# Kernel optimization log

Measured on AMD Instinct MI355X. Metric: run time of the kernel, lower is better.

Reference implementation:

```python
import jax, jax.numpy as jnp
import numpy as np

N, E, D, H, C = 50000, 1600000, 256, 8, 32

def setup_inputs() -> dict:
    key = jax.random.key(0)
    ks = jax.random.split(key, 7)
    feat = jax.random.normal(ks[0], (N, D), dtype=jnp.float32)
    edge_weight = jax.random.uniform(ks[1], (E,), dtype=jnp.float32)
    W_lin = jax.random.normal(ks[2], (D, H * C), dtype=jnp.float32) * (1.0 / np.sqrt(D))
    att_l = jax.random.normal(ks[3], (1, H, C), dtype=jnp.float32) * (1.0 / np.sqrt(H))
    att_r = jax.random.normal(ks[4], (1, H, C), dtype=jnp.float32) * (1.0 / np.sqrt(H))
    W_res = jax.random.normal(ks[5], (D, H * C), dtype=jnp.float32) * (1.0 / np.sqrt(D))
    edge_index = jax.random.randint(ks[6], (2, E), 0, N, dtype=jnp.int32)
    return {"feat": feat, "edge_weight": edge_weight, "W_lin": W_lin,
            "att_l": att_l, "att_r": att_r, "W_res": W_res, "edge_index": edge_index}

def reference(feat, edge_weight, W_lin, att_l, att_r, W_res, edge_index):
    n_nodes = feat.shape[0]
    h, c = att_l.shape[1], att_l.shape[2]
    src, dst = edge_index[0], edge_index[1]
    # node projection: [N, H, C]
    x = (feat @ W_lin).reshape(n_nodes, h, c)
    alpha_l = (x * att_l).sum(-1)  # [N, H]
    alpha_r = (x * att_r).sum(-1)  # [N, H]
    # per-edge scores [E, H]
    alpha = alpha_l[src] + alpha_r[dst]
    alpha = edge_weight[:, None] * alpha
    alpha = jnp.where(alpha > 0, alpha, 0.2 * alpha)  # leaky_relu(0.2)
    # segment softmax over destination nodes
    amax = jax.lax.stop_gradient(jax.ops.segment_max(alpha, dst, num_segments=n_nodes))
    ex = jnp.exp(alpha - amax[dst])
    denom = jax.ops.segment_sum(ex, dst, num_segments=n_nodes)
    coeff = ex / (denom[dst] + 1e-16)  # [E, H]
    # weighted message aggregation
    msg = x[src] * coeff[:, :, None]  # [E, H, C]
    agg = jax.ops.segment_sum(msg, dst, num_segments=n_nodes)  # [N, H, C]
    out = jax.nn.elu(agg).reshape(n_nodes, h * c)
    out = out + feat @ W_res  # residual
    return out
```

## Files before the change

### kernel.cpp

```cpp
#include <hip/hip_runtime.h>
#include <stdint.h>

#define D_DIM 256
#define NPAD  640
#define NSH   8

typedef __bf16 bf16x8 __attribute__((ext_vector_type(8)));
typedef float  f32x4  __attribute__((ext_vector_type(4)));

__device__ __forceinline__ float bf2f(unsigned short u) {
  union { unsigned int i; float f; } cv; cv.i = ((unsigned int)u) << 16; return cv.f;
}
__device__ __forceinline__ unsigned short f2bf(float f) {
  union { float f; unsigned int i; } cv; cv.f = f;
  unsigned int i = cv.i;
  unsigned int lsb = (i >> 16) & 1u;
  i += 0x7fffu + lsb;
  return (unsigned short)(i >> 16);
}
__device__ __forceinline__ void gld16(const void* gptr, void* lptr) {
  __builtin_amdgcn_global_load_lds(
      (const __attribute__((address_space(1))) unsigned int*)gptr,
      (__attribute__((address_space(3))) unsigned int*)lptr, 16, 0, 0);
}

__global__ __launch_bounds__(256) void setup_fused(
    const float* __restrict__ feat, unsigned short* __restrict__ fb,
    const float* __restrict__ W_lin, const float* __restrict__ W_res,
    const float* __restrict__ att_l, const float* __restrict__ att_r,
    unsigned short* __restrict__ Bt, int nelem, int nb_hist, int nb_cvt,
    const int* __restrict__ dst, int* __restrict__ cntS, int* __restrict__ rank,
    int E, int Np) {
  int bid = blockIdx.x, t = threadIdx.x;
  if (bid < nb_hist) {
    int base = bid * 2048 + t;
    #pragma unroll
    for (int u = 0; u < 8; ++u) {
      int e = base + u * 256;
      if (e < E) {
        int d = dst[e];
        rank[e] = atomicAdd(&cntS[(e & (NSH - 1)) * Np + d], 1);
      }
    }
    return;
  }
  bid -= nb_hist;
  if (bid < nb_cvt) {
    int i = (bid * 256 + t) * 8;
    if (i >= nelem) return;
    float4 v0 = *(const float4*)(feat + i);
    float4 v1 = *(const float4*)(feat + i + 4);
    ushort4 a, b;
    a.x = f2bf(v0.x); a.y = f2bf(v0.y); a.z = f2bf(v0.z); a.w = f2bf(v0.w);
    b.x = f2bf(v1.x); b.y = f2bf(v1.y); b.z = f2bf(v1.z); b.w = f2bf(v1.w);
    *(ushort4*)(fb + i) = a;
    *(ushort4*)(fb + i + 4) = b;
  } else {
    int idx = (bid - nb_cvt) * 256 + t;
    int n = idx >> 8, k = idx & 255;
    float v = 0.f;
    if (n < 256) v = W_lin[k * 256 + n];
    else if (n < 512) v = W_res[k * 256 + (n - 256)];
    else if (n < 520) {
      int h = n - 512; float s = 0.f;
      #pragma unroll
      for (int c = 0; c < 32; ++c) s += W_lin[k * 256 + h * 32 + c] * att_l[h * 32 + c];
      v = s;
    } else if (n < 528) {
      int h = n - 520; float s = 0.f;
      #pragma unroll
      for (int c = 0; c < 32; ++c) s += W_lin[k * 256 + h * 32 + c] * att_r[h * 32 + c];
      v = s;
    }
    Bt[idx] = f2bf(v);
  }
}

__global__ __launch_bounds__(256) void scan_partial(const int* __restrict__ cntS,
                                                    int* __restrict__ bsum, int N, int Np) {
  __shared__ int s[256];
  int t = threadIdx.x;
  int i = blockIdx.x * 256 + t;
  int v = 0;
  if (i < N) {
    #pragma unroll
    for (int sh = 0; sh < NSH; ++sh) v += cntS[sh * Np + i];
  }
  s[t] = v;
  __syncthreads();
  for (int off = 128; off > 0; off >>= 1) {
    if (t < off) s[t] += s[t + off];
    __syncthreads();
  }
  if (t == 0) bsum[blockIdx.x] = s[0];
}

__global__ __launch_bounds__(256) void scan_apply(const int* __restrict__ cntS,
                                                  const int* __restrict__ bsum,
                                                  int* __restrict__ row_ptr,
                                                  int* __restrict__ soffA, int N, int Np) {
  __shared__ int red[256];
  __shared__ int s[256];
  int t = threadIdx.x;
  int b = blockIdx.x;
  int acc = 0;
  for (int j = t; j < b; j += 256) acc += bsum[j];
  red[t] = acc;
  __syncthreads();
  for (int off = 128; off > 0; off >>= 1) {
    if (t < off) red[t] += red[t + off];
    __syncthreads();
  }
  int base = red[0];

  int i = b * 256 + t;
  int c[NSH]; int v = 0;
  if (i < N) {
    #pragma unroll
    for (int sh = 0; sh < NSH; ++sh) { c[sh] = cntS[sh * Np + i]; v += c[sh]; }
  }
  s[t] = v;
  __syncthreads();
  for (int off = 1; off < 256; off <<= 1) {
    int u = (t >= off) ? s[t - off] : 0;
    __syncthreads();
    s[t] += u;
    __syncthreads();
  }
  int excl = base + s[t] - v;
  if (i < N) {
    row_ptr[i] = excl;
    int run = excl;
    #pragma unroll
    for (int sh = 0; sh < NSH; ++sh) { soffA[sh * Np + i] = run; run += c[sh]; }
    if (i == N - 1) row_ptr[N] = excl + v;
  }
}

__global__ __launch_bounds__(256) void gemm_kernel(
    const unsigned short* __restrict__ A,
    const unsigned short* __restrict__ Bt,
    float* __restrict__ out, unsigned short* __restrict__ xbf,
    float* __restrict__ alpha_l, float* __restrict__ alpha_r, int M, int gx) {
  __shared__ unsigned short As[128 * 64];
  __shared__ unsigned short Bs[128 * 64];

  int tid  = threadIdx.x;
  int w    = tid >> 6, lane = tid & 63;

  int nwg  = (int)gridDim.x;
  int q    = nwg >> 3, r = nwg & 7;
  int xcd  = (int)blockIdx.x & 7, j = (int)blockIdx.x >> 3;
  int wg   = (xcd < r ? xcd * (q + 1) : r * (q + 1) + (xcd - r) * q) + j;

  int nbn  = NPAD / 128;
  int bm   = (wg / nbn) * 128, bn = (wg % nbn) * 128;
  int wm   = (w & 1) * 64, wn = (w >> 1) * 64;
  int l16  = lane & 15, quad = lane >> 4;

  f32x4 acc[4][4] = {};

  int sr8     = lane >> 3;
  int koff_sw = (((lane & 7) ^ sr8) * 8);

  for (int k0 = 0; k0 < 256; k0 += 64) {
    #pragma unroll
    for (int jj = 0; jj < 4; ++jj) {
      int rbase = w * 32 + jj * 8;
      int rga = bm + rbase + sr8; if (rga > M - 1) rga = M - 1;
      gld16(A  + (size_t)rga * 256 + k0 + koff_sw, &As[rbase * 64]);
      gld16(Bt + (size_t)(bn + rbase + sr8) * 256 + k0 + koff_sw, &Bs[rbase * 64]);
    }
    __syncthreads();
    #pragma unroll
    for (int kk = 0; kk < 64; kk += 32) {
      bf16x8 a[4], b[4];
      #pragma unroll
      for (int mi = 0; mi < 4; ++mi) {
        int rr = wm + mi * 16 + l16;
        int col = (kk * 2 + quad * 16) ^ ((rr & 7) << 4);
        a[mi] = *(const bf16x8*)((const char*)&As[rr * 64] + col);
      }
      #pragma unroll
      for (int ni = 0; ni < 4; ++ni) {
        int rr = wn + ni * 16 + l16;
        int col = (kk * 2 + quad * 16) ^ ((rr & 7) << 4);
        b[ni] = *(const bf16x8*)((const char*)&Bs[rr * 64] + col);
      }
      #pragma unroll
      for (int mi = 0; mi < 4; ++mi)
        #pragma unroll
        for (int ni = 0; ni < 4; ++ni)
          acc[mi][ni] = __builtin_amdgcn_mfma_f32_16x16x32_bf16(a[mi], b[ni], acc[mi][ni], 0, 0, 0);
    }
    __syncthreads();
  }

  #pragma unroll
  for (int mi = 0; mi < 4; ++mi) {
    #pragma unroll
    for (int rr = 0; rr < 4; ++rr) {
      int row = bm + wm + mi * 16 + quad * 4 + rr;
      if (row >= M) continue;
      #pragma unroll
      for (int ni = 0; ni < 4; ++ni) {
        int n = bn + wn + ni * 16 + l16;
        float v = acc[mi][ni][rr];
        if (n < 256)      xbf[(size_t)row * 256 + n] = f2bf(v);
        else if (n < 512) out[(size_t)row * 256 + (n - 256)] = v;
        else if (n < 520) alpha_l[row * 8 + (n - 512)] = v;
        else if (n < 528) alpha_r[row * 8 + (n - 520)] = v;
      }
    }
  }
}

__global__ __launch_bounds__(256) void scatter_kernel(
    const int* __restrict__ eidx, const float* __restrict__ ew,
    const int* __restrict__ soffA, const int* __restrict__ rank,
    int2* __restrict__ pairs, int E, int Np) {
  int e = blockIdx.x * 256 + threadIdx.x;
  if (e < E) {
    int d = eidx[E + e];
    int pos = soffA[(e & (NSH - 1)) * Np + d] + rank[e];
    int2 p; p.x = eidx[e]; p.y = __float_as_int(ew[e]);
    pairs[pos] = p;
  }
}

__global__ __launch_bounds__(256) void agg_kernel(
    const int* __restrict__ row_ptr, const int2* __restrict__ pairs,
    const float* __restrict__ alpha_l, const float* __restrict__ alpha_r,
    const unsigned short* __restrict__ xbf, float* __restrict__ out,
    int node_base, int node_lim) {
  __shared__ float red[2][64][6];
  int nin  = threadIdx.x >> 7;
  int wv   = (threadIdx.x >> 6) & 1;
  int lane = threadIdx.x & 63;
  int node = node_base + blockIdx.x * 2 + nin;
  bool active = node < node_lim;
  int h  = lane >> 3;
  int cb = lane << 2;

  float l = 0.f, ac0 = 0.f, ac1 = 0.f, ac2 = 0.f, ac3 = 0.f;

  if (active) {
    int beg = row_ptr[node], end = row_ptr[node + 1];
    if (beg < end) {
      float arv = alpha_r[node * 8 + h];
      int last = end - 1;
      const unsigned short* xb = xbf + cb;
      for (int jg = beg + wv * 4; jg < end; jg += 8) {
        int2 q[4];
        #pragma unroll
        for (int u = 0; u < 4; ++u) {
          int t = jg + u; t = (t < last) ? t : last;
          q[u] = pairs[t];
        }
        float al[4];
        #pragma unroll
        for (int u = 0; u < 4; ++u) al[u] = alpha_l[(size_t)q[u].x * 8 + h];
        ushort4 xv[4];
        #pragma unroll
        for (int u = 0; u < 4; ++u)
          xv[u] = *(const ushort4*)(xb + ((size_t)q[u].x << 8));
        #pragma unroll
        for (int u = 0; u < 4; ++u) {
          float a = __int_as_float(q[u].y) * (al[u] + arv);
          a = (a > 0.f) ? a : 0.2f * a;
          float p = __expf(a);
          p = (jg + u < end) ? p : 0.f;
          l += p;
          ac0 = fmaf(p, bf2f(xv[u].x), ac0);
          ac1 = fmaf(p, bf2f(xv[u].y), ac1);
          ac2 = fmaf(p, bf2f(xv[u].z), ac2);
          ac3 = fmaf(p, bf2f(xv[u].w), ac3);
        }
      }
    }
  }

  if (wv == 1) {
    red[nin][lane][0] = l;
    red[nin][lane][1] = ac0; red[nin][lane][2] = ac1;
    red[nin][lane][3] = ac2; red[nin][lane][4] = ac3;
  }
  __syncthreads();
  if (active && wv == 0) {
    l   += red[nin][lane][0];
    ac0 += red[nin][lane][1]; ac1 += red[nin][lane][2];
    ac2 += red[nin][lane][3]; ac3 += red[nin][lane][4];
    float r = 1.0f / (l + 1e-16f);
    float o0 = ac0 * r, o1 = ac1 * r, o2 = ac2 * r, o3 = ac3 * r;
    o0 = (o0 > 0.f) ? o0 : expm1f(o0);
    o1 = (o1 > 0.f) ? o1 : expm1f(o1);
    o2 = (o2 > 0.f) ? o2 : expm1f(o2);
    o3 = (o3 > 0.f) ? o3 : expm1f(o3);
    float4* op = (float4*)(out + ((size_t)node << 8) + cb);
    float4 res = *op;
    res.x += o0; res.y += o1; res.z += o2; res.w += o3;
    *op = res;
  }
}

extern "C" void kernel_launch(void* const* d_in, const int* in_sizes, int n_in,
                              void* d_out, int out_size, void* d_ws, size_t ws_size,
                              hipStream_t stream) {
  const float* feat  = (const float*)d_in[0];
  const float* ew    = (const float*)d_in[1];
  const float* W_lin = (const float*)d_in[2];
  const float* att_l = (const float*)d_in[3];
  const float* att_r = (const float*)d_in[4];
  const float* W_res = (const float*)d_in[5];
  const int*   eidx  = (const int*)d_in[6];
  float* out = (float*)d_out;

  int N = in_sizes[0] / D_DIM;
  int E = in_sizes[1];
  int Np = (N + 255) & ~255;

  char* p = (char*)d_ws;
  auto alloc = [&](size_t bytes) {
    char* r = p; p += (bytes + 255) & ~(size_t)255; return r;
  };
  unsigned short* xbf  = (unsigned short*)alloc((size_t)N * 256 * 2);
  unsigned short* fb   = (unsigned short*)alloc((size_t)N * 256 * 2);
  float* alpha_l       = (float*)alloc((size_t)N * 8 * 4);
  float* alpha_r       = (float*)alloc((size_t)N * 8 * 4);
  unsigned short* Bt   = (unsigned short*)alloc((size_t)NPAD * D_DIM * 2);
  int*   row_ptr       = (int*)alloc((size_t)(N + 1) * 4);
  int*   cntS          = (int*)alloc((size_t)NSH * Np * 4);
  int*   soffA         = (int*)alloc((size_t)NSH * Np * 4);
  int*   rank          = (int*)alloc((size_t)E * 4);
  int*   bsum          = (int*)alloc(1024);
  int2*  pairs_sep     = (int2*)alloc((size_t)E * 8);
  bool sep_ok = ((size_t)((char*)(pairs_sep + E) - (char*)d_ws) <= ws_size);
  int2* pairs = sep_ok ? pairs_sep : (int2*)fb;

  int nb      = (N + 255) / 256;
  int nb_cvt  = (N * 256 / 8 + 255) / 256;
  int nb_prep = NPAD * D_DIM / 256;
  int nb_hist = (E + 2047) / 2048;
  int nb_scat = (E + 255) / 256;
  int gx = (N + 127) / 128;
  int gemm_blocks = gx * (NPAD / 128);

  hipMemsetAsync(cntS, 0, (size_t)NSH * Np * 4, stream);

  setup_fused<<<nb_hist + nb_cvt + nb_prep, 256, 0, stream>>>(
      feat, fb, W_lin, W_res, att_l, att_r, Bt, N * 256, nb_hist, nb_cvt,
      eidx + E, cntS, rank, E, Np);

  gemm_kernel<<<gemm_blocks, 256, 0, stream>>>(
      fb, Bt, out, xbf, alpha_l, alpha_r, N, gx);

  scan_partial<<<nb, 256, 0, stream>>>(cntS, bsum, N, Np);
  scan_apply<<<nb, 256, 0, stream>>>(cntS, bsum, row_ptr, soffA, N, Np);

  scatter_kernel<<<nb_scat, 256, 0, stream>>>(eidx, ew, soffA, rank, pairs, E, Np);

  int Nh = ((N / 2) + 1) & ~1;
  if (Nh > N) Nh = N;
  int blocksA = (Nh + 1) / 2;
  int blocksB = (N - Nh + 1) / 2;
  if (blocksA > 0)
    agg_kernel<<<blocksA, 256, 0, stream>>>(row_ptr, pairs, alpha_l, alpha_r, xbf, out, 0, Nh);
  if (blocksB > 0)
    agg_kernel<<<blocksB, 256, 0, stream>>>(row_ptr, pairs, alpha_l, alpha_r, xbf, out, Nh, N);
}
```

Before: 402.3 us.

## Move edge histogram into GEMM epilogue and merge split aggregation launches

The per-destination edge histogram (atomic counts and ranks) moves out of the setup kernel and runs at the end of each GEMM block, over a chunk of edges sized so the GEMM grid covers all edges. The atomic work can then overlap with the memory- and compute-bound GEMM tail instead of running as separate blocks ahead of it. The two half-range aggregation launches are also merged into one launch over all nodes, saving a launch. The risk is longer GEMM blocks, plus atomic traffic contending with the GEMM stores.

```diff
diff --git a/kernel.cpp b/kernel.cpp
--- a/kernel.cpp
+++ b/kernel.cpp
@@ -24,27 +24,12 @@
       (__attribute__((address_space(3))) unsigned int*)lptr, 16, 0, 0);
 }
 
-__global__ __launch_bounds__(256) void setup_fused(
+__global__ __launch_bounds__(256) void setup_cvt_prep(
     const float* __restrict__ feat, unsigned short* __restrict__ fb,
     const float* __restrict__ W_lin, const float* __restrict__ W_res,
     const float* __restrict__ att_l, const float* __restrict__ att_r,
-    unsigned short* __restrict__ Bt, int nelem, int nb_hist, int nb_cvt,
-    const int* __restrict__ dst, int* __restrict__ cntS, int* __restrict__ rank,
-    int E, int Np) {
+    unsigned short* __restrict__ Bt, int nelem, int nb_cvt) {
   int bid = blockIdx.x, t = threadIdx.x;
-  if (bid < nb_hist) {
-    int base = bid * 2048 + t;
-    #pragma unroll
-    for (int u = 0; u < 8; ++u) {
-      int e = base + u * 256;
-      if (e < E) {
-        int d = dst[e];
-        rank[e] = atomicAdd(&cntS[(e & (NSH - 1)) * Np + d], 1);
-      }
-    }
-    return;
-  }
-  bid -= nb_hist;
   if (bid < nb_cvt) {
     int i = (bid * 256 + t) * 8;
     if (i >= nelem) return;
@@ -141,7 +126,9 @@
     const unsigned short* __restrict__ A,
     const unsigned short* __restrict__ Bt,
     float* __restrict__ out, unsigned short* __restrict__ xbf,
-    float* __restrict__ alpha_l, float* __restrict__ alpha_r, int M, int gx) {
+    float* __restrict__ alpha_l, float* __restrict__ alpha_r, int M, int gx,
+    const int* __restrict__ dst, int* __restrict__ cntS, int* __restrict__ rank,
+    int E, int Np, int echunk) {
   __shared__ unsigned short As[128 * 64];
   __shared__ unsigned short Bs[128 * 64];
 
@@ -212,6 +199,13 @@
         else if (n < 528) alpha_r[row * 8 + (n - 520)] = v;
       }
     }
+  }
+
+  int ebase = (int)blockIdx.x * echunk;
+  int elim  = ebase + echunk; if (elim > E) elim = E;
+  for (int e = ebase + tid; e < elim; e += 256) {
+    int d = dst[e];
+    rank[e] = atomicAdd(&cntS[(e & (NSH - 1)) * Np + d], 1);
   }
 }
 
@@ -231,14 +225,13 @@
 __global__ __launch_bounds__(256) void agg_kernel(
     const int* __restrict__ row_ptr, const int2* __restrict__ pairs,
     const float* __restrict__ alpha_l, const float* __restrict__ alpha_r,
-    const unsigned short* __restrict__ xbf, float* __restrict__ out,
-    int node_base, int node_lim) {
+    const unsigned short* __restrict__ xbf, float* __restrict__ out, int N) {
   __shared__ float red[2][64][6];
   int nin  = threadIdx.x >> 7;
   int wv   = (threadIdx.x >> 6) & 1;
   int lane = threadIdx.x & 63;
-  int node = node_base + blockIdx.x * 2 + nin;
-  bool active = node < node_lim;
+  int node = blockIdx.x * 2 + nin;
+  bool active = node < N;
   int h  = lane >> 3;
   int cb = lane << 2;
 
@@ -340,31 +333,24 @@
   int nb      = (N + 255) / 256;
   int nb_cvt  = (N * 256 / 8 + 255) / 256;
   int nb_prep = NPAD * D_DIM / 256;
-  int nb_hist = (E + 2047) / 2048;
   int nb_scat = (E + 255) / 256;
   int gx = (N + 127) / 128;
   int gemm_blocks = gx * (NPAD / 128);
+  int echunk = (E + gemm_blocks - 1) / gemm_blocks;
 
   hipMemsetAsync(cntS, 0, (size_t)NSH * Np * 4, stream);
 
-  setup_fused<<<nb_hist + nb_cvt + nb_prep, 256, 0, stream>>>(
-      feat, fb, W_lin, W_res, att_l, att_r, Bt, N * 256, nb_hist, nb_cvt,
-      eidx + E, cntS, rank, E, Np);
+  setup_cvt_prep<<<nb_cvt + nb_prep, 256, 0, stream>>>(
+      feat, fb, W_lin, W_res, att_l, att_r, Bt, N * 256, nb_cvt);
 
   gemm_kernel<<<gemm_blocks, 256, 0, stream>>>(
-      fb, Bt, out, xbf, alpha_l, alpha_r, N, gx);
+      fb, Bt, out, xbf, alpha_l, alpha_r, N, gx,
+      eidx + E, cntS, rank, E, Np, echunk);
 
   scan_partial<<<nb, 256, 0, stream>>>(cntS, bsum, N, Np);
   scan_apply<<<nb, 256, 0, stream>>>(cntS, bsum, row_ptr, soffA, N, Np);
 
   scatter_kernel<<<nb_scat, 256, 0, stream>>>(eidx, ew, soffA, rank, pairs, E, Np);
 
-  int Nh = ((N / 2) + 1) & ~1;
-  if (Nh > N) Nh = N;
-  int blocksA = (Nh + 1) / 2;
-  int blocksB = (N - Nh + 1) / 2;
-  if (blocksA > 0)
-    agg_kernel<<<blocksA, 256, 0, stream>>>(row_ptr, pairs, alpha_l, alpha_r, xbf, out, 0, Nh);
-  if (blocksB > 0)
-    agg_kernel<<<blocksB, 256, 0, stream>>>(row_ptr, pairs, alpha_l, alpha_r, xbf, out, Nh, N);
-}
+  agg_kernel<<<(N + 1) / 2, 256, 0, stream>>>(row_ptr, pairs, alpha_l, alpha_r, xbf, out, N);
+}
```

After: 400.3 us. No clear change (-0.5%).
